# Kernel tuning notes

Hardware: AMD Instinct MI355X
Metric: run time of the kernel (lower is better)

The kernel has to match this reference:

```python
import jax, jax.numpy as jnp
import numpy as np

# Config (matches init_kwargs)
S = 8            # num_seqs
LQ = 256         # query tokens per sequence (num_tokens = S*LQ = 2048)
SEQ = 2048       # kv seq_len per sequence
BLK = 16         # block size
NBLK_PER_SEQ = SEQ // BLK   # 128 = max_num_blocks_per_seq
NUM_BLKS = S * NBLK_PER_SEQ # 1024
HQ = 32          # num_query_heads
HKV = 8          # num_kv_heads
G = HQ // HKV    # queries per kv head (GQA group)
D = 128          # head_size
WINDOW = 1024    # sliding_window
SCALE = 1.0 / float(np.sqrt(D))


def setup_inputs() -> dict:
    key = jax.random.key(0)
    k1, k2, k3 = jax.random.split(key, 3)
    query = jax.random.normal(k1, (S * LQ, HQ, D), jnp.float32)
    key_cache = jax.random.normal(k2, (NUM_BLKS, BLK, HKV, D), jnp.float32)
    value_cache = jax.random.normal(k3, (NUM_BLKS, BLK, HKV, D), jnp.float32)
    # each sequence owns a contiguous run of blocks; all indices valid (>=0)
    block_tables = jnp.arange(NUM_BLKS, dtype=jnp.int32).reshape(S, NBLK_PER_SEQ)
    seq_lens = jnp.full((S,), SEQ, dtype=jnp.int32)
    query_start_len = (jnp.arange(S + 1, dtype=jnp.int32) * LQ)
    return dict(query=query, key_cache=key_cache, value_cache=value_cache,
                block_tables=block_tables, seq_lens=seq_lens,
                query_start_len=query_start_len)


def reference(query, key_cache, value_cache, block_tables, seq_lens, query_start_len):
    # query: [S*LQ, HQ, D] -> [S, LQ, HKV, G, D]
    q = query.reshape(S, LQ, HKV, G, D)
    # paged KV gather: [S, NBLK_PER_SEQ] -> [S, NBLK_PER_SEQ, BLK, HKV, D] -> [S, SEQ, HKV, D]
    K = key_cache[block_tables].reshape(S, SEQ, HKV, D)
    V = value_cache[block_tables].reshape(S, SEQ, HKV, D)
    # attention scores: [S, HKV, G, LQ, SEQ]
    scores = jnp.einsum('sqhgd,skhd->shgqk', q, K) * SCALE
    # causal + sliding-window mask over absolute positions
    ctx = SEQ - LQ  # context_len (same for all seqs here)
    qpos = ctx + jnp.arange(LQ)          # [LQ] absolute query positions
    kpos = jnp.arange(SEQ)               # [SEQ] absolute key positions
    valid = (kpos[None, :] <= qpos[:, None]) & \
            (qpos[:, None] - kpos[None, :] < WINDOW)   # [LQ, SEQ]
    neg_inf = jnp.asarray(-jnp.inf, scores.dtype)
    scores = jnp.where(valid[None, None, None, :, :], scores, neg_inf)
    probs = jax.nn.softmax(scores, axis=-1)
    # output: [S, LQ, HKV, G, D] -> [S*LQ, HQ, D]
    out = jnp.einsum('shgqk,skhd->sqhgd', probs, V)
    return out.reshape(S * LQ, HQ, D)
```

## Files before the change

### kernel.cpp

```cpp
#include <hip/hip_runtime.h>
#include <stdint.h>

typedef __attribute__((ext_vector_type(8))) short short8;
typedef __attribute__((ext_vector_type(4))) float floatx4;
typedef __attribute__((ext_vector_type(4))) unsigned int uint4v;

#define NSEQ 8
#define BLKSZ 16
#define NBLK_PER_SEQ 128
#define HQN 32
#define HKVN 8
#define GQ 4
#define HD 128
#define WINDOW 1024
#define SCALE 0.08838834764831845f

#define QB 32
#define KVB 64
#define KROW 136
#define VROW 72

#define MFMA16 __builtin_amdgcn_mfma_f32_16x16x32_bf16

static __device__ __forceinline__ unsigned int pack2bf(float lo, float hi) {
    unsigned int a = __builtin_bit_cast(unsigned int, lo) + 0x8000u;
    unsigned int b = __builtin_bit_cast(unsigned int, hi) + 0x8000u;
    return __builtin_amdgcn_perm(b, a, 0x07060302u);
}

__global__ __launch_bounds__(256, 2)
void attn_fwd(const float* __restrict__ qg,
              const float* __restrict__ kg,
              const float* __restrict__ vg,
              const int* __restrict__ bt,
              const int* __restrict__ seqlens,
              const int* __restrict__ qsl,
              float* __restrict__ outg)
{
    __shared__ __align__(16) short Klds[KVB][KROW];
    __shared__ __align__(16) short Vt[HD][VROW];

    const int tid  = threadIdx.x;
    const int wave = tid >> 6;
    const int lane = tid & 63;
    const int l15  = lane & 15;
    const int lg   = lane >> 4;

    const int b  = blockIdx.x;
    const int h  = b & 7;
    const int qt = (b >> 3) & 7;
    const int s  = b >> 6;
    const int q0 = qt * QB;

    const int qstart = qsl[s];
    const int numq   = qsl[s + 1] - qstart;
    const int slen   = seqlens[s];
    const int ctx    = slen - numq;
    const int hq     = h * GQ + wave;

    short8 qf[2][4];
    #pragma unroll
    for (int nq = 0; nq < 2; ++nq) {
        const float* qrow = qg + ((size_t)(qstart + q0 + nq * 16 + l15) * HQN + hq) * HD;
        #pragma unroll
        for (int kt = 0; kt < 4; ++kt) {
            floatx4 f0 = *(const floatx4*)(qrow + kt * 32 + lg * 8);
            floatx4 f1 = *(const floatx4*)(qrow + kt * 32 + lg * 8 + 4);
            uint4v w;
            w[0] = pack2bf(f0[0] * SCALE, f0[1] * SCALE);
            w[1] = pack2bf(f0[2] * SCALE, f0[3] * SCALE);
            w[2] = pack2bf(f1[0] * SCALE, f1[1] * SCALE);
            w[3] = pack2bf(f1[2] * SCALE, f1[3] * SCALE);
            qf[nq][kt] = __builtin_bit_cast(short8, w);
        }
    }

    floatx4 oacc[2][8];
    #pragma unroll
    for (int nq = 0; nq < 2; ++nq)
        #pragma unroll
        for (int dt = 0; dt < 8; ++dt)
            oacc[nq][dt] = (floatx4){0.f, 0.f, 0.f, 0.f};

    float mrun[2] = {-INFINITY, -INFINITY};
    float lrun[2] = {0.f, 0.f};

    int lo = ctx + q0 - WINDOW + 1; if (lo < 0) lo = 0;
    int hi = ctx + q0 + QB - 1;     if (hi > slen - 1) hi = slen - 1;
    const int t0 = lo / KVB, t1 = hi / KVB;

    const int srow = tid >> 3;
    const int sd0  = (tid & 7) * 16;
    const int k2   = tid & 31;
    const int d0v  = (tid >> 5) * 16;

    floatx4 fk[8], fv[8];

    {
        const int kv0 = t0 * KVB;
        #pragma unroll
        for (int p = 0; p < 2; ++p) {
            const int kvp = kv0 + p * 32 + srow;
            const int blk = bt[s * NBLK_PER_SEQ + (kvp >> 4)];
            const float* src = kg + (((size_t)blk * BLKSZ + (kvp & 15)) * HKVN + h) * HD + sd0;
            fk[p*4+0] = *(const floatx4*)(src);
            fk[p*4+1] = *(const floatx4*)(src + 4);
            fk[p*4+2] = *(const floatx4*)(src + 8);
            fk[p*4+3] = *(const floatx4*)(src + 12);
        }
        const int kvv = kv0 + 2 * k2;
        const int blk = bt[s * NBLK_PER_SEQ + (kvv >> 4)];
        const float* src = vg + (((size_t)blk * BLKSZ + (kvv & 15)) * HKVN + h) * HD + d0v;
        #pragma unroll
        for (int j = 0; j < 4; ++j) {
            fv[j]     = *(const floatx4*)(src + j * 4);
            fv[4 + j] = *(const floatx4*)(src + (size_t)HKVN * HD + j * 4);
        }
    }

    for (int t = t0; t <= t1; ++t) {
        const int kv0 = t * KVB;
        __syncthreads();

        #pragma unroll
        for (int p = 0; p < 2; ++p) {
            const int row = p * 32 + srow;
            uint4v w;
            w[0] = pack2bf(fk[p*4+0][0], fk[p*4+0][1]);
            w[1] = pack2bf(fk[p*4+0][2], fk[p*4+0][3]);
            w[2] = pack2bf(fk[p*4+1][0], fk[p*4+1][1]);
            w[3] = pack2bf(fk[p*4+1][2], fk[p*4+1][3]);
            *(uint4v*)&Klds[row][sd0] = w;
            w[0] = pack2bf(fk[p*4+2][0], fk[p*4+2][1]);
            w[1] = pack2bf(fk[p*4+2][2], fk[p*4+2][3]);
            w[2] = pack2bf(fk[p*4+3][0], fk[p*4+3][1]);
            w[3] = pack2bf(fk[p*4+3][2], fk[p*4+3][3]);
            *(uint4v*)&Klds[row][sd0 + 8] = w;
        }
        #pragma unroll
        for (int i = 0; i < 16; ++i) {
            *(unsigned int*)&Vt[d0v + i][2 * k2] =
                pack2bf(fv[i >> 2][i & 3], fv[4 + (i >> 2)][i & 3]);
        }
        __syncthreads();

        floatx4 sacc[2][4];
        #pragma unroll
        for (int nq = 0; nq < 2; ++nq)
            #pragma unroll
            for (int m2 = 0; m2 < 4; ++m2)
                sacc[nq][m2] = (floatx4){0.f, 0.f, 0.f, 0.f};
        #pragma unroll
        for (int kt = 0; kt < 4; ++kt) {
            #pragma unroll
            for (int m2 = 0; m2 < 4; ++m2) {
                short8 kf = *(const short8*)&Klds[m2 * 16 + l15][kt * 32 + lg * 8];
                sacc[0][m2] = MFMA16(kf, qf[0][kt], sacc[0][m2], 0, 0, 0);
                sacc[1][m2] = MFMA16(kf, qf[1][kt], sacc[1][m2], 0, 0, 0);
            }
        }

        if (t < t1) {
            const int kv0n = kv0 + KVB;
            #pragma unroll
            for (int p = 0; p < 2; ++p) {
                const int kvp = kv0n + p * 32 + srow;
                const int blk = bt[s * NBLK_PER_SEQ + (kvp >> 4)];
                const float* src = kg + (((size_t)blk * BLKSZ + (kvp & 15)) * HKVN + h) * HD + sd0;
                fk[p*4+0] = *(const floatx4*)(src);
                fk[p*4+1] = *(const floatx4*)(src + 4);
                fk[p*4+2] = *(const floatx4*)(src + 8);
                fk[p*4+3] = *(const floatx4*)(src + 12);
            }
            const int kvv = kv0n + 2 * k2;
            const int blk = bt[s * NBLK_PER_SEQ + (kvv >> 4)];
            const float* src = vg + (((size_t)blk * BLKSZ + (kvv & 15)) * HKVN + h) * HD + d0v;
            #pragma unroll
            for (int j = 0; j < 4; ++j) {
                fv[j]     = *(const floatx4*)(src + j * 4);
                fv[4 + j] = *(const floatx4*)(src + (size_t)HKVN * HD + j * 4);
            }
        }

        const bool interior = (kv0 >= ctx + q0 - (WINDOW - QB)) &&
                              (kv0 + KVB - 1 <= ctx + q0);
        short8 pfv[2][2];
        const int srcA = ((lg & 1) << 5) + l15;
        const int srcB = srcA + 16;
        const bool hiSel = (lg >> 1) != 0;
        #pragma unroll
        for (int nq = 0; nq < 2; ++nq) {
            const int qpos = ctx + q0 + nq * 16 + l15;
            float sv[4][4];
            #pragma unroll
            for (int m2 = 0; m2 < 4; ++m2) {
                #pragma unroll
                for (int r = 0; r < 4; ++r) {
                    float x = sacc[nq][m2][r];
                    if (!interior) {
                        const int kpos = kv0 + m2 * 16 + lg * 4 + r;
                        const bool valid = (kpos <= qpos) && (qpos - kpos < WINDOW);
                        x = valid ? x : -INFINITY;
                    }
                    sv[m2][r] = x;
                }
            }
            float rmax = -INFINITY;
            #pragma unroll
            for (int m2 = 0; m2 < 4; ++m2)
                #pragma unroll
                for (int r = 0; r < 4; ++r)
                    rmax = fmaxf(rmax, sv[m2][r]);
            rmax = fmaxf(rmax, __shfl_xor(rmax, 16));
            rmax = fmaxf(rmax, __shfl_xor(rmax, 32));
            const float mold = mrun[nq];
            const bool defer = __all(rmax <= mold + 8.0f);
            const float mnew = defer ? mold : fmaxf(mold, rmax);
            const float alpha = defer ? 1.0f
                : ((mold == -INFINITY) ? ((mnew == -INFINITY) ? 1.0f : 0.0f)
                                       : __expf(mold - mnew));
            const bool dead = (mnew == -INFINITY);
            float rsum = 0.f;
            #pragma unroll
            for (int m2 = 0; m2 < 4; ++m2)
                #pragma unroll
                for (int r = 0; r < 4; ++r) {
                    float e = dead ? 0.f : __expf(sv[m2][r] - mnew);
                    sv[m2][r] = e;
                    rsum += e;
                }
            rsum += __shfl_xor(rsum, 16);
            rsum += __shfl_xor(rsum, 32);
            lrun[nq] = lrun[nq] * alpha + rsum;
            mrun[nq] = mnew;
            if (!defer) {
                #pragma unroll
                for (int dt = 0; dt < 8; ++dt) {
                    oacc[nq][dt][0] *= alpha; oacc[nq][dt][1] *= alpha;
                    oacc[nq][dt][2] *= alpha; oacc[nq][dt][3] *= alpha;
                }
            }
            unsigned int pk0[4], pk1[4];
            #pragma unroll
            for (int m2 = 0; m2 < 4; ++m2) {
                pk0[m2] = pack2bf(sv[m2][0], sv[m2][1]);
                pk1[m2] = pack2bf(sv[m2][2], sv[m2][3]);
            }
            #pragma unroll
            for (int ks = 0; ks < 2; ++ks) {
                unsigned int a0 = (unsigned int)__shfl((int)pk0[2*ks],   srcA, 64);
                unsigned int a1 = (unsigned int)__shfl((int)pk0[2*ks+1], srcA, 64);
                unsigned int b0 = (unsigned int)__shfl((int)pk1[2*ks],   srcA, 64);
                unsigned int b1 = (unsigned int)__shfl((int)pk1[2*ks+1], srcA, 64);
                unsigned int c0 = (unsigned int)__shfl((int)pk0[2*ks],   srcB, 64);
                unsigned int c1 = (unsigned int)__shfl((int)pk0[2*ks+1], srcB, 64);
                unsigned int d0 = (unsigned int)__shfl((int)pk1[2*ks],   srcB, 64);
                unsigned int d1 = (unsigned int)__shfl((int)pk1[2*ks+1], srcB, 64);
                uint4v w;
                w[0] = hiSel ? a1 : a0;
                w[1] = hiSel ? b1 : b0;
                w[2] = hiSel ? c1 : c0;
                w[3] = hiSel ? d1 : d0;
                pfv[ks][nq] = __builtin_bit_cast(short8, w);
            }
        }

        #pragma unroll
        for (int ks = 0; ks < 2; ++ks) {
            #pragma unroll
            for (int dt = 0; dt < 8; ++dt) {
                short8 vfn = *(const short8*)&Vt[dt * 16 + l15][ks * 32 + lg * 8];
                oacc[0][dt] = MFMA16(vfn, pfv[ks][0], oacc[0][dt], 0, 0, 0);
                oacc[1][dt] = MFMA16(vfn, pfv[ks][1], oacc[1][dt], 0, 0, 0);
            }
        }
    }

    #pragma unroll
    for (int nq = 0; nq < 2; ++nq) {
        const float inv = 1.0f / lrun[nq];
        float* orow = outg + ((size_t)(qstart + q0 + nq * 16 + l15) * HQN + hq) * HD + lg * 4;
        #pragma unroll
        for (int dt = 0; dt < 8; ++dt) {
            floatx4 o = oacc[nq][dt];
            o[0] *= inv; o[1] *= inv; o[2] *= inv; o[3] *= inv;
            *(floatx4*)(orow + dt * 16) = o;
        }
    }
}

extern "C" void kernel_launch(void* const* d_in, const int* in_sizes, int n_in,
                              void* d_out, int out_size, void* d_ws, size_t ws_size,
                              hipStream_t stream) {
    const float* q  = (const float*)d_in[0];
    const float* k  = (const float*)d_in[1];
    const float* v  = (const float*)d_in[2];
    const int* btp  = (const int*)d_in[3];
    const int* sl   = (const int*)d_in[4];
    const int* qs   = (const int*)d_in[5];
    float* out      = (float*)d_out;

    attn_fwd<<<dim3(NSEQ * HKVN * 8), 256, 0, stream>>>(q, k, v, btp, sl, qs, out);
}
```

Before: 96.99 us.

## Double-buffer K/V LDS tiles with 32-row KV blocks and single barrier

Halves the KV tile to 32 keys and double-buffers the K and transposed-V shared-memory tiles so each iteration needs only one __syncthreads. The next tile's global loads are issued right after the current tile is written to LDS. The smaller tile lowers register pressure, since prefetch buffers are halved. In exchange it doubles the loop trip count, so per-iteration softmax, shuffle and barrier overhead is paid twice as often with less MFMA work per barrier.

```diff
diff --git a/kernel.cpp b/kernel.cpp
--- a/kernel.cpp
+++ b/kernel.cpp
@@ -16,9 +16,9 @@
 #define SCALE 0.08838834764831845f
 
 #define QB 32
-#define KVB 64
+#define KVB 32
 #define KROW 136
-#define VROW 72
+#define VROW 40
 
 #define MFMA16 __builtin_amdgcn_mfma_f32_16x16x32_bf16
 
@@ -37,12 +37,12 @@
               const int* __restrict__ qsl,
               float* __restrict__ outg)
 {
-    __shared__ __align__(16) short Klds[KVB][KROW];
-    __shared__ __align__(16) short Vt[HD][VROW];
+    __shared__ __align__(16) short Klds[2][KVB][KROW];
+    __shared__ __align__(16) short Vt[2][HD][VROW];
 
     const int tid  = threadIdx.x;
+    const int lane = tid & 63;
     const int wave = tid >> 6;
-    const int lane = tid & 63;
     const int l15  = lane & 15;
     const int lg   = lane >> 4;
 
@@ -91,109 +91,82 @@
 
     const int srow = tid >> 3;
     const int sd0  = (tid & 7) * 16;
-    const int k2   = tid & 31;
-    const int d0v  = (tid >> 5) * 16;
-
-    floatx4 fk[8], fv[8];
-
-    {
-        const int kv0 = t0 * KVB;
-        #pragma unroll
-        for (int p = 0; p < 2; ++p) {
-            const int kvp = kv0 + p * 32 + srow;
-            const int blk = bt[s * NBLK_PER_SEQ + (kvp >> 4)];
-            const float* src = kg + (((size_t)blk * BLKSZ + (kvp & 15)) * HKVN + h) * HD + sd0;
-            fk[p*4+0] = *(const floatx4*)(src);
-            fk[p*4+1] = *(const floatx4*)(src + 4);
-            fk[p*4+2] = *(const floatx4*)(src + 8);
-            fk[p*4+3] = *(const floatx4*)(src + 12);
-        }
-        const int kvv = kv0 + 2 * k2;
-        const int blk = bt[s * NBLK_PER_SEQ + (kvv >> 4)];
-        const float* src = vg + (((size_t)blk * BLKSZ + (kvv & 15)) * HKVN + h) * HD + d0v;
-        #pragma unroll
-        for (int j = 0; j < 4; ++j) {
-            fv[j]     = *(const floatx4*)(src + j * 4);
-            fv[4 + j] = *(const floatx4*)(src + (size_t)HKVN * HD + j * 4);
-        }
-    }
-
+    const int k2   = tid & 15;
+    const int d0v  = (tid >> 4) * 8;
+
+    floatx4 fk[4], fv[4];
+
+#define LOAD_TILE(kv0_) {                                                            \
+        const int kvp = (kv0_) + srow;                                               \
+        const int blk = bt[s * NBLK_PER_SEQ + (kvp >> 4)];                           \
+        const float* src = kg + (((size_t)blk * BLKSZ + (kvp & 15)) * HKVN + h) * HD + sd0; \
+        fk[0] = *(const floatx4*)(src);                                              \
+        fk[1] = *(const floatx4*)(src + 4);                                          \
+        fk[2] = *(const floatx4*)(src + 8);                                          \
+        fk[3] = *(const floatx4*)(src + 12);                                         \
+        const int kvv = (kv0_) + 2 * k2;                                             \
+        const int blkv = bt[s * NBLK_PER_SEQ + (kvv >> 4)];                          \
+        const float* vsrc = vg + (((size_t)blkv * BLKSZ + (kvv & 15)) * HKVN + h) * HD + d0v; \
+        fv[0] = *(const floatx4*)(vsrc);                                             \
+        fv[1] = *(const floatx4*)(vsrc + 4);                                         \
+        fv[2] = *(const floatx4*)(vsrc + (size_t)HKVN * HD);                         \
+        fv[3] = *(const floatx4*)(vsrc + (size_t)HKVN * HD + 4);                     \
+    }
+
+    LOAD_TILE(t0 * KVB);
+
+    int cur = 0;
     for (int t = t0; t <= t1; ++t) {
         const int kv0 = t * KVB;
+
+        {
+            uint4v w;
+            w[0] = pack2bf(fk[0][0], fk[0][1]);
+            w[1] = pack2bf(fk[0][2], fk[0][3]);
+            w[2] = pack2bf(fk[1][0], fk[1][1]);
+            w[3] = pack2bf(fk[1][2], fk[1][3]);
+            *(uint4v*)&Klds[cur][srow][sd0] = w;
+            w[0] = pack2bf(fk[2][0], fk[2][1]);
+            w[1] = pack2bf(fk[2][2], fk[2][3]);
+            w[2] = pack2bf(fk[3][0], fk[3][1]);
+            w[3] = pack2bf(fk[3][2], fk[3][3]);
+            *(uint4v*)&Klds[cur][srow][sd0 + 8] = w;
+            #pragma unroll
+            for (int i = 0; i < 8; ++i) {
+                *(unsigned int*)&Vt[cur][d0v + i][2 * k2] =
+                    pack2bf(fv[i >> 2][i & 3], fv[2 + (i >> 2)][i & 3]);
+            }
+        }
+
+        if (t < t1) LOAD_TILE(kv0 + KVB);
+
         __syncthreads();
 
-        #pragma unroll
-        for (int p = 0; p < 2; ++p) {
-            const int row = p * 32 + srow;
-            uint4v w;
-            w[0] = pack2bf(fk[p*4+0][0], fk[p*4+0][1]);
-            w[1] = pack2bf(fk[p*4+0][2], fk[p*4+0][3]);
-            w[2] = pack2bf(fk[p*4+1][0], fk[p*4+1][1]);
-            w[3] = pack2bf(fk[p*4+1][2], fk[p*4+1][3]);
-            *(uint4v*)&Klds[row][sd0] = w;
-            w[0] = pack2bf(fk[p*4+2][0], fk[p*4+2][1]);
-            w[1] = pack2bf(fk[p*4+2][2], fk[p*4+2][3]);
-            w[2] = pack2bf(fk[p*4+3][0], fk[p*4+3][1]);
-            w[3] = pack2bf(fk[p*4+3][2], fk[p*4+3][3]);
-            *(uint4v*)&Klds[row][sd0 + 8] = w;
-        }
-        #pragma unroll
-        for (int i = 0; i < 16; ++i) {
-            *(unsigned int*)&Vt[d0v + i][2 * k2] =
-                pack2bf(fv[i >> 2][i & 3], fv[4 + (i >> 2)][i & 3]);
-        }
-        __syncthreads();
-
-        floatx4 sacc[2][4];
-        #pragma unroll
-        for (int nq = 0; nq < 2; ++nq)
-            #pragma unroll
-            for (int m2 = 0; m2 < 4; ++m2)
-                sacc[nq][m2] = (floatx4){0.f, 0.f, 0.f, 0.f};
+        floatx4 sacc[2][2];
+        sacc[0][0] = (floatx4){0.f,0.f,0.f,0.f}; sacc[0][1] = (floatx4){0.f,0.f,0.f,0.f};
+        sacc[1][0] = (floatx4){0.f,0.f,0.f,0.f}; sacc[1][1] = (floatx4){0.f,0.f,0.f,0.f};
         #pragma unroll
         for (int kt = 0; kt < 4; ++kt) {
             #pragma unroll
-            for (int m2 = 0; m2 < 4; ++m2) {
-                short8 kf = *(const short8*)&Klds[m2 * 16 + l15][kt * 32 + lg * 8];
+            for (int m2 = 0; m2 < 2; ++m2) {
+                short8 kf = *(const short8*)&Klds[cur][m2 * 16 + l15][kt * 32 + lg * 8];
                 sacc[0][m2] = MFMA16(kf, qf[0][kt], sacc[0][m2], 0, 0, 0);
                 sacc[1][m2] = MFMA16(kf, qf[1][kt], sacc[1][m2], 0, 0, 0);
             }
         }
 
-        if (t < t1) {
-            const int kv0n = kv0 + KVB;
-            #pragma unroll
-            for (int p = 0; p < 2; ++p) {
-                const int kvp = kv0n + p * 32 + srow;
-                const int blk = bt[s * NBLK_PER_SEQ + (kvp >> 4)];
-                const float* src = kg + (((size_t)blk * BLKSZ + (kvp & 15)) * HKVN + h) * HD + sd0;
-                fk[p*4+0] = *(const floatx4*)(src);
-                fk[p*4+1] = *(const floatx4*)(src + 4);
-                fk[p*4+2] = *(const floatx4*)(src + 8);
-                fk[p*4+3] = *(const floatx4*)(src + 12);
-            }
-            const int kvv = kv0n + 2 * k2;
-            const int blk = bt[s * NBLK_PER_SEQ + (kvv >> 4)];
-            const float* src = vg + (((size_t)blk * BLKSZ + (kvv & 15)) * HKVN + h) * HD + d0v;
-            #pragma unroll
-            for (int j = 0; j < 4; ++j) {
-                fv[j]     = *(const floatx4*)(src + j * 4);
-                fv[4 + j] = *(const floatx4*)(src + (size_t)HKVN * HD + j * 4);
-            }
-        }
-
         const bool interior = (kv0 >= ctx + q0 - (WINDOW - QB)) &&
                               (kv0 + KVB - 1 <= ctx + q0);
-        short8 pfv[2][2];
+        short8 pfv[2];
         const int srcA = ((lg & 1) << 5) + l15;
         const int srcB = srcA + 16;
         const bool hiSel = (lg >> 1) != 0;
         #pragma unroll
         for (int nq = 0; nq < 2; ++nq) {
             const int qpos = ctx + q0 + nq * 16 + l15;
-            float sv[4][4];
-            #pragma unroll
-            for (int m2 = 0; m2 < 4; ++m2) {
+            float sv[2][4];
+            #pragma unroll
+            for (int m2 = 0; m2 < 2; ++m2) {
                 #pragma unroll
                 for (int r = 0; r < 4; ++r) {
                     float x = sacc[nq][m2][r];
@@ -207,7 +180,7 @@
             }
             float rmax = -INFINITY;
             #pragma unroll
-            for (int m2 = 0; m2 < 4; ++m2)
+            for (int m2 = 0; m2 < 2; ++m2)
                 #pragma unroll
                 for (int r = 0; r < 4; ++r)
                     rmax = fmaxf(rmax, sv[m2][r]);
@@ -222,7 +195,7 @@
             const bool dead = (mnew == -INFINITY);
             float rsum = 0.f;
             #pragma unroll
-            for (int m2 = 0; m2 < 4; ++m2)
+            for (int m2 = 0; m2 < 2; ++m2)
                 #pragma unroll
                 for (int r = 0; r < 4; ++r) {
                     float e = dead ? 0.f : __expf(sv[m2][r] - mnew);
@@ -240,41 +213,40 @@
                     oacc[nq][dt][2] *= alpha; oacc[nq][dt][3] *= alpha;
                 }
             }
-            unsigned int pk0[4], pk1[4];
-            #pragma unroll
-            for (int m2 = 0; m2 < 4; ++m2) {
+            unsigned int pk0[2], pk1[2];
+            #pragma unroll
+            for (int m2 = 0; m2 < 2; ++m2) {
                 pk0[m2] = pack2bf(sv[m2][0], sv[m2][1]);
                 pk1[m2] = pack2bf(sv[m2][2], sv[m2][3]);
             }
-            #pragma unroll
-            for (int ks = 0; ks < 2; ++ks) {
-                unsigned int a0 = (unsigned int)__shfl((int)pk0[2*ks],   srcA, 64);
-                unsigned int a1 = (unsigned int)__shfl((int)pk0[2*ks+1], srcA, 64);
-                unsigned int b0 = (unsigned int)__shfl((int)pk1[2*ks],   srcA, 64);
-                unsigned int b1 = (unsigned int)__shfl((int)pk1[2*ks+1], srcA, 64);
-                unsigned int c0 = (unsigned int)__shfl((int)pk0[2*ks],   srcB, 64);
-                unsigned int c1 = (unsigned int)__shfl((int)pk0[2*ks+1], srcB, 64);
-                unsigned int d0 = (unsigned int)__shfl((int)pk1[2*ks],   srcB, 64);
-                unsigned int d1 = (unsigned int)__shfl((int)pk1[2*ks+1], srcB, 64);
+            {
+                unsigned int a0 = (unsigned int)__shfl((int)pk0[0], srcA, 64);
+                unsigned int a1 = (unsigned int)__shfl((int)pk0[1], srcA, 64);
+                unsigned int b0 = (unsigned int)__shfl((int)pk1[0], srcA, 64);
+                unsigned int b1 = (unsigned int)__shfl((int)pk1[1], srcA, 64);
+                unsigned int c0 = (unsigned int)__shfl((int)pk0[0], srcB, 64);
+                unsigned int c1 = (unsigned int)__shfl((int)pk0[1], srcB, 64);
+                unsigned int d0 = (unsigned int)__shfl((int)pk1[0], srcB, 64);
+                unsigned int d1 = (unsigned int)__shfl((int)pk1[1], srcB, 64);
                 uint4v w;
                 w[0] = hiSel ? a1 : a0;
                 w[1] = hiSel ? b1 : b0;
                 w[2] = hiSel ? c1 : c0;
                 w[3] = hiSel ? d1 : d0;
-                pfv[ks][nq] = __builtin_bit_cast(short8, w);
-            }
-        }
-
-        #pragma unroll
-        for (int ks = 0; ks < 2; ++ks) {
-            #pragma unroll
-            for (int dt = 0; dt < 8; ++dt) {
-                short8 vfn = *(const short8*)&Vt[dt * 16 + l15][ks * 32 + lg * 8];
-                oacc[0][dt] = MFMA16(vfn, pfv[ks][0], oacc[0][dt], 0, 0, 0);
-                oacc[1][dt] = MFMA16(vfn, pfv[ks][1], oacc[1][dt], 0, 0, 0);
-            }
-        }
-    }
+                pfv[nq] = __builtin_bit_cast(short8, w);
+            }
+        }
+
+        #pragma unroll
+        for (int dt = 0; dt < 8; ++dt) {
+            short8 vfn = *(const short8*)&Vt[cur][dt * 16 + l15][lg * 8];
+            oacc[0][dt] = MFMA16(vfn, pfv[0], oacc[0][dt], 0, 0, 0);
+            oacc[1][dt] = MFMA16(vfn, pfv[1], oacc[1][dt], 0, 0, 0);
+        }
+
+        cur ^= 1;
+    }
+#undef LOAD_TILE
 
     #pragma unroll
     for (int nq = 0; nq < 2; ++nq) {
```

New measurement: 92.88 us. 4.2% less time.
